# Optimization experiments

Measured on AMD Instinct MI355X. Metric: run time of the kernel, lower is better.

The kernel has to match this reference:

```python
import jax, jax.numpy as jnp
import numpy as np

B, J, D, H = 4096, 17, 512, 8
DK = D // H  # 64
NEG = jnp.float32(-9e15)


def _build_adj_mask():
    # Human3.6M 17-joint skeleton (parent indices), symmetric + self-loops,
    # matching SemGCN's adj>0 mask (adj_mx_from_edges adds identity).
    parents = np.array([-1, 0, 1, 2, 0, 4, 5, 0, 7, 8, 9, 8, 11, 12, 8, 14, 15])
    A = np.eye(J, dtype=np.float32)
    for c, p in enumerate(parents):
        if p >= 0:
            A[c, p] = 1.0
            A[p, c] = 1.0
    rows, cols = np.nonzero(A)
    return rows.astype(np.int32), cols.astype(np.int32)


def setup_inputs() -> dict:
    key = jax.random.key(0)
    ks = jax.random.split(key, 16)
    s = 0.02
    rows, cols = _build_adj_mask()
    return {
        "src": jax.random.normal(ks[0], (B, J, D), jnp.float32),
        # per-head Q/K/V Linears, stacked over heads: [H, D, DK]
        "Wq": jax.random.normal(ks[1], (H, D, DK), jnp.float32) * s,
        "bq": jnp.zeros((H, DK), jnp.float32),
        "Wk": jax.random.normal(ks[2], (H, D, DK), jnp.float32) * s,
        "bk": jnp.zeros((H, DK), jnp.float32),
        "Wv": jax.random.normal(ks[3], (H, D, DK), jnp.float32) * s,
        "bv": jnp.zeros((H, DK), jnp.float32),
        # output projection of MultiHeadAttention: [H*DK, D]
        "Wo": jax.random.normal(ks[4], (H * DK, D), jnp.float32) * s,
        "bo": jnp.zeros((D,), jnp.float32),
        "ln1_g": jnp.ones((D,), jnp.float32),
        "ln1_b": jnp.zeros((D,), jnp.float32),
        # SemGraphConv: two weight matrices [2, D, D], edge logits e, bias
        "W_gcn": jax.random.normal(ks[5], (2, D, D), jnp.float32) * s,
        "e_gcn": jax.random.normal(ks[6], (rows.shape[0],), jnp.float32),
        "b_gcn": jnp.zeros((D,), jnp.float32),
        "ln2_g": jnp.ones((D,), jnp.float32),
        "ln2_b": jnp.zeros((D,), jnp.float32),
        "mask_rows": jnp.asarray(rows),
        "mask_cols": jnp.asarray(cols),
    }


def _layernorm(x, g, b, eps=1e-5):
    mu = jnp.mean(x, axis=-1, keepdims=True)
    var = jnp.var(x, axis=-1, keepdims=True)
    return (x - mu) * jax.lax.rsqrt(var + eps) * g + b


def _forward(src, Wq, bq, Wk, bk, Wv, bv, Wo, bo, ln1_g, ln1_b,
             W_gcn, e_gcn, b_gcn, ln2_g, ln2_b, mask_rows, mask_cols):
    # --- multi-head attention (all heads vectorized) ---
    q = jnp.einsum('bjd,hde->bhje', src, Wq) + bq[None, :, None, :]
    k = jnp.einsum('bjd,hde->bhje', src, Wk) + bk[None, :, None, :]
    v = jnp.einsum('bjd,hde->bhje', src, Wv) + bv[None, :, None, :]
    scale = jnp.float32(DK) ** 0.5  # q.size(-1) ** 0.5
    att = jax.nn.softmax(jnp.einsum('bhje,bhke->bhjk', q, k) / scale, axis=-1)
    o = jnp.einsum('bhjk,bhke->bhje', att, v)          # [B,H,J,DK]
    o = o.transpose(0, 2, 1, 3).reshape(B, J, H * DK)  # concat over heads
    attn_out = o @ Wo + bo
    x = _layernorm(src + attn_out, ln1_g, ln1_b)

    # --- SemGraphConv ---
    h0 = x @ W_gcn[0]
    h1 = x @ W_gcn[1]
    logits = jnp.full((J, J), NEG, jnp.float32).at[mask_rows, mask_cols].set(e_gcn)
    A = jax.nn.softmax(logits, axis=1)                 # [J,J]
    I = jnp.eye(J, dtype=jnp.float32)
    gcn = jnp.einsum('jk,bkd->bjd', A * I, h0) + jnp.einsum('jk,bkd->bjd', A * (1.0 - I), h1)
    gcn = gcn + b_gcn
    return _layernorm(x + gcn, ln2_g, ln2_b)


def reference(src, Wq, bq, Wk, bk, Wv, bv, Wo, bo, ln1_g, ln1_b,
              W_gcn, e_gcn, b_gcn, ln2_g, ln2_b, mask_rows, mask_cols):
    return _forward(src, Wq, bq, Wk, bk, Wv, bv, Wo, bo, ln1_g, ln1_b,
                    W_gcn, e_gcn, b_gcn, ln2_g, ln2_b, mask_rows, mask_cols)
```

## Files before the change

kernel.cpp:

```cpp
#include <hip/hip_runtime.h>


typedef __attribute__((ext_vector_type(4))) float floatx4;
typedef __attribute__((ext_vector_type(8))) short short8;

#define AS1 __attribute__((address_space(1)))
#define AS3 __attribute__((address_space(3)))

__device__ __forceinline__ float bf2f(unsigned short u) {
  union { unsigned int i; float f; } x;
  x.i = ((unsigned int)u) << 16;
  return x.f;
}

__device__ __forceinline__ unsigned short f2bf(float f) {
  union { float f; unsigned int i; } x;
  x.f = f;
  unsigned int r = x.i + 0x7fffu + ((x.i >> 16) & 1u);
  return (unsigned short)(r >> 16);
}

__device__ __forceinline__ void unpack8(uint4 u, float* f) {
  unsigned int uu[4] = {u.x, u.y, u.z, u.w};
#pragma unroll
  for (int i = 0; i < 4; ++i) {
    f[2 * i]     = bf2f((unsigned short)(uu[i] & 0xffffu));
    f[2 * i + 1] = bf2f((unsigned short)(uu[i] >> 16));
  }
}

__device__ __forceinline__ uint4 pack8(const float* f) {
  unsigned int uu[4];
#pragma unroll
  for (int i = 0; i < 4; ++i)
    uu[i] = (unsigned int)f2bf(f[2 * i]) | ((unsigned int)f2bf(f[2 * i + 1]) << 16);
  uint4 u; u.x = uu[0]; u.y = uu[1]; u.z = uu[2]; u.w = uu[3];
  return u;
}

__device__ __forceinline__ float wave_sum(float v) {
#pragma unroll
  for (int m = 1; m < 64; m <<= 1) v += __shfl_xor(v, m, 64);
  return v;
}

__device__ __forceinline__ void gload_lds16(const unsigned short* g, AS3 char* l) {
  __builtin_amdgcn_global_load_lds((const AS1 void*)g, (AS3 void*)l, 16, 0, 0);
}

__global__ __launch_bounds__(256) void convert_src(
    const float* __restrict__ in, unsigned short* __restrict__ out) {
  const size_t i = ((size_t)blockIdx.x * 256 + threadIdx.x) * 8;
  const float4 a = *(const float4*)(in + i);
  const float4 b = *(const float4*)(in + i + 4);
  const float f[8] = {a.x, a.y, a.z, a.w, b.x, b.y, b.z, b.w};
  *(uint4*)(out + i) = pack8(f);
}

__device__ __forceinline__ void stgA(const unsigned short* a0, size_t gTh,
                                     AS3 char* L, int ldsW, int bb, int kt,
                                     int kh) {
  gload_lds16(a0 + gTh + kt * 64 + kh * 32,
              L + bb * 32768 + kh * 16384 + ldsW);
  gload_lds16(a0 + gTh + 65536 + kt * 64 + kh * 32,
              L + bb * 32768 + kh * 16384 + 8192 + ldsW);
}
__device__ __forceinline__ void stgB(const unsigned short* b0, size_t gTh,
                                     AS3 char* L, int ldsW, int bb, int kt,
                                     int kh) {
  gload_lds16(b0 + gTh + kt * 64 + kh * 32,
              L + 65536 + bb * 32768 + kh * 16384 + ldsW);
  gload_lds16(b0 + gTh + 65536 + kt * 64 + kh * 32,
              L + 65536 + bb * 32768 + kh * 16384 + 8192 + ldsW);
}

template <int BB>
__device__ __forceinline__ void kt_step(
    int kt, const char* Lr, AS3 char* L,
    const unsigned short* a0, const unsigned short* b0, size_t gTh, int ldsW,
    int aBase, int bBase, floatx4 (&acc)[8][4]) {
  constexpr int base = BB * 32768;
  short8 afL[4], afH[4], bf[4];

#pragma unroll
  for (int i = 0; i < 4; ++i)
    afL[i] = *(const short8*)(Lr + base + aBase + i * 1024);
#pragma unroll
  for (int j = 0; j < 4; ++j)
    bf[j] = *(const short8*)(Lr + base + bBase + j * 1024);
  if (kt < 7) stgA(a0, gTh, L, ldsW, BB ^ 1, kt + 1, 1);
  __builtin_amdgcn_s_barrier();
  asm volatile("s_waitcnt lgkmcnt(0)" ::: "memory");
  __builtin_amdgcn_sched_barrier(0);
  __builtin_amdgcn_s_setprio(1);
#pragma unroll
  for (int i = 0; i < 4; ++i)
#pragma unroll
    for (int j = 0; j < 4; ++j)
      acc[i][j] = __builtin_amdgcn_mfma_f32_16x16x32_bf16(afL[i], bf[j], acc[i][j], 0, 0, 0);
  __builtin_amdgcn_s_setprio(0);
  __builtin_amdgcn_s_barrier();

#pragma unroll
  for (int i = 0; i < 4; ++i)
    afH[i] = *(const short8*)(Lr + base + aBase + 4096 + i * 1024);
  if (kt < 7) stgB(b0, gTh, L, ldsW, BB ^ 1, kt + 1, 1);
  __builtin_amdgcn_s_barrier();
  asm volatile("s_waitcnt lgkmcnt(0)" ::: "memory");
  __builtin_amdgcn_sched_barrier(0);
  __builtin_amdgcn_s_setprio(1);
#pragma unroll
  for (int i = 0; i < 4; ++i)
#pragma unroll
    for (int j = 0; j < 4; ++j)
      acc[4 + i][j] = __builtin_amdgcn_mfma_f32_16x16x32_bf16(afH[i], bf[j], acc[4 + i][j], 0, 0, 0);
  __builtin_amdgcn_s_setprio(0);
  if (kt < 7) asm volatile("s_waitcnt vmcnt(8)" ::: "memory");
  else        asm volatile("s_waitcnt vmcnt(0)" ::: "memory");
  __builtin_amdgcn_sched_barrier(0);
  __builtin_amdgcn_s_barrier();

#pragma unroll
  for (int i = 0; i < 4; ++i)
    afL[i] = *(const short8*)(Lr + base + 16384 + aBase + i * 1024);
#pragma unroll
  for (int j = 0; j < 4; ++j)
    bf[j] = *(const short8*)(Lr + base + 16384 + bBase + j * 1024);
  if (kt < 6) stgA(a0, gTh, L, ldsW, BB, kt + 2, 0);
  __builtin_amdgcn_s_barrier();
  asm volatile("s_waitcnt lgkmcnt(0)" ::: "memory");
  __builtin_amdgcn_sched_barrier(0);
  __builtin_amdgcn_s_setprio(1);
#pragma unroll
  for (int i = 0; i < 4; ++i)
#pragma unroll
    for (int j = 0; j < 4; ++j)
      acc[i][j] = __builtin_amdgcn_mfma_f32_16x16x32_bf16(afL[i], bf[j], acc[i][j], 0, 0, 0);
  __builtin_amdgcn_s_setprio(0);
  __builtin_amdgcn_s_barrier();

#pragma unroll
  for (int i = 0; i < 4; ++i)
    afH[i] = *(const short8*)(Lr + base + 16384 + aBase + 4096 + i * 1024);
  if (kt < 6) stgB(b0, gTh, L, ldsW, BB, kt + 2, 0);
  __builtin_amdgcn_s_barrier();
  asm volatile("s_waitcnt lgkmcnt(0)" ::: "memory");
  __builtin_amdgcn_sched_barrier(0);
  __builtin_amdgcn_s_setprio(1);
#pragma unroll
  for (int i = 0; i < 4; ++i)
#pragma unroll
    for (int j = 0; j < 4; ++j)
      acc[4 + i][j] = __builtin_amdgcn_mfma_f32_16x16x32_bf16(afH[i], bf[j], acc[4 + i][j], 0, 0, 0);
  __builtin_amdgcn_s_setprio(0);
  if (kt < 6)       asm volatile("s_waitcnt vmcnt(8)" ::: "memory");
  else if (kt == 6) asm volatile("s_waitcnt vmcnt(4)" ::: "memory");
  __builtin_amdgcn_sched_barrier(0);
  __builtin_amdgcn_s_barrier();
}

__global__ __launch_bounds__(512, 2) void gemm_bt(
    const unsigned short* __restrict__ A,
    const unsigned short* __restrict__ BT,
    const float* __restrict__ bias,
    unsigned short* __restrict__ C, int N) {
  __shared__ char LDSR[131072];
  const int t = threadIdx.x;
  const int wave = t >> 6, lane = t & 63;
  const int wm = wave >> 2, wn = wave & 3;
  const int e = lane & 15, g = lane >> 4;

  const int nTN = N >> 8;
  const int q8 = gridDim.x >> 3;
  const int lin = ((int)blockIdx.x & 7) * q8 + ((int)blockIdx.x >> 3);
  const int tm = lin / nTN;
  const int tn = lin - tm * nTN;
  const long rowBase = (long)tm * 256;
  const long colBase = (long)tn * 256;

  const unsigned short* a0 = A + (size_t)rowBase * 512;
  const unsigned short* b0 = BT + (size_t)colBase * 512;

  const size_t gTh = (size_t)(t >> 2) * 512 +
                     (size_t)(((t & 3) ^ ((t >> 3) & 3))) * 8;
  AS3 char* L = (AS3 char*)LDSR;
  const int ldsW = wave * 1024;

  const int swz16 = ((g ^ ((e >> 1) & 3)) << 4);
  const char* Lr = LDSR;
  const int aBase = wm * 8192 + e * 64 + swz16;
  const int bBase = 65536 + wn * 4096 + e * 64 + swz16;

  floatx4 acc[8][4];
#pragma unroll
  for (int i = 0; i < 8; ++i)
#pragma unroll
    for (int j = 0; j < 4; ++j) acc[i][j] = (floatx4){0.f, 0.f, 0.f, 0.f};

  stgA(a0, gTh, L, ldsW, 0, 0, 0); stgB(b0, gTh, L, ldsW, 0, 0, 0);
  stgA(a0, gTh, L, ldsW, 0, 0, 1); stgB(b0, gTh, L, ldsW, 0, 0, 1);
  stgA(a0, gTh, L, ldsW, 1, 1, 0); stgB(b0, gTh, L, ldsW, 1, 1, 0);
  asm volatile("s_waitcnt vmcnt(8)" ::: "memory");
  __builtin_amdgcn_sched_barrier(0);
  __builtin_amdgcn_s_barrier();

#pragma unroll 1
  for (int ktp = 0; ktp < 4; ++ktp) {
    kt_step<0>(2 * ktp,     Lr, L, a0, b0, gTh, ldsW, aBase, bBase, acc);
    kt_step<1>(2 * ktp + 1, Lr, L, a0, b0, gTh, ldsW, aBase, bBase, acc);
  }

  asm volatile("s_waitcnt vmcnt(0) lgkmcnt(0)" ::: "memory");
  __builtin_amdgcn_sched_barrier(0);

  const int q4 = g << 2;
#pragma unroll
  for (int mf = 0; mf < 8; ++mf) {
    const long rowa = rowBase + wm * 128 + mf * 16 + q4;
#pragma unroll
    for (int nf = 0; nf < 4; ++nf) {
      const long col = colBase + wn * 64 + nf * 16 + e;
      const float badd = bias ? bias[col] : 0.f;
#pragma unroll
      for (int r = 0; r < 4; ++r)
        C[(size_t)(rowa + r) * N + col] = f2bf(acc[mf][nf][r] + badd);
    }
  }
}

__global__ __launch_bounds__(256) void attn_kernel(
    const unsigned short* __restrict__ qkv, unsigned short* __restrict__ o) {
  __shared__ unsigned short Vl[4][17][76];
  const int t = threadIdx.x;
  const int wave = t >> 6, lane = t & 63;
  const int wid = blockIdx.x * 4 + wave;
  const int b = wid >> 3, h = wid & 7;
  const int e = lane & 15, g = lane >> 4;

  const unsigned short* base = qkv + (size_t)b * 17 * 1536 + h * 64;

  unsigned short (*V)[76] = Vl[wave];
  for (int c = lane; c < 136; c += 64) {
    const int kk = c >> 3, e0 = (c & 7) << 3;
    const uint4 u = *(const uint4*)(base + (size_t)kk * 1536 + 1024 + e0);
    *(uint2*)&V[kk][e0]     = make_uint2(u.x, u.y);
    *(uint2*)&V[kk][e0 + 4] = make_uint2(u.z, u.w);
  }

  const int ko = g << 3;
  const unsigned short* qrow  = base + (size_t)e * 1536;
  const unsigned short* row16 = base + (size_t)16 * 1536;
  const short8 Q0  = *(const short8*)(qrow + ko);
  const short8 Q1  = *(const short8*)(qrow + 32 + ko);
  const short8 K0  = *(const short8*)(qrow + 512 + ko);
  const short8 K1  = *(const short8*)(qrow + 512 + 32 + ko);
  const short8 Qb0 = *(const short8*)(row16 + ko);
  const short8 Qb1 = *(const short8*)(row16 + 32 + ko);
  const short8 Kb0 = *(const short8*)(row16 + 512 + ko);
  const short8 Kb1 = *(const short8*)(row16 + 512 + 32 + ko);

  floatx4 sT[2][2];
#pragma unroll
  for (int i = 0; i < 2; ++i)
#pragma unroll
    for (int j = 0; j < 2; ++j) sT[i][j] = (floatx4){0.f, 0.f, 0.f, 0.f};
  sT[0][0] = __builtin_amdgcn_mfma_f32_16x16x32_bf16(K0, Q0, sT[0][0], 0, 0, 0);
  sT[0][0] = __builtin_amdgcn_mfma_f32_16x16x32_bf16(K1, Q1, sT[0][0], 0, 0, 0);
  sT[0][1] = __builtin_amdgcn_mfma_f32_16x16x32_bf16(K0, Qb0, sT[0][1], 0, 0, 0);
  sT[0][1] = __builtin_amdgcn_mfma_f32_16x16x32_bf16(K1, Qb1, sT[0][1], 0, 0, 0);
  sT[1][0] = __builtin_amdgcn_mfma_f32_16x16x32_bf16(Kb0, Q0, sT[1][0], 0, 0, 0);
  sT[1][0] = __builtin_amdgcn_mfma_f32_16x16x32_bf16(Kb1, Q1, sT[1][0], 0, 0, 0);
  sT[1][1] = __builtin_amdgcn_mfma_f32_16x16x32_bf16(Kb0, Qb0, sT[1][1], 0, 0, 0);
  sT[1][1] = __builtin_amdgcn_mfma_f32_16x16x32_bf16(Kb1, Qb1, sT[1][1], 0, 0, 0);

  short8 PA[2];
#pragma unroll
  for (int ni = 0; ni < 2; ++ni) {
    float v[4];
#pragma unroll
    for (int r = 0; r < 4; ++r) v[r] = sT[0][ni][r] * 0.125f;
    const float v16 = sT[1][ni][0] * 0.125f;
    float m = fmaxf(fmaxf(v[0], v[1]), fmaxf(v[2], v[3]));
    if (g == 0) m = fmaxf(m, v16);
    m = fmaxf(m, __shfl_xor(m, 16, 64));
    m = fmaxf(m, __shfl_xor(m, 32, 64));
    float p[4], sum = 0.f;
#pragma unroll
    for (int r = 0; r < 4; ++r) { p[r] = __expf(v[r] - m); sum += p[r]; }
    float p16 = (g == 0) ? __expf(v16 - m) : 0.f;
    sum += p16;
    sum += __shfl_xor(sum, 16, 64);
    sum += __shfl_xor(sum, 32, 64);
    const float inv = 1.f / sum;
#pragma unroll
    for (int r = 0; r < 4; ++r) p[r] *= inv;
    p16 *= inv;

    const unsigned int lo = (unsigned int)f2bf(p[0]) | ((unsigned int)f2bf(p[1]) << 16);
    const unsigned int hi = (unsigned int)f2bf(p[2]) | ((unsigned int)f2bf(p[3]) << 16);
    const unsigned int w16 = (unsigned int)f2bf(p16);

    const int colsrc = ni ? 0 : e;
    const int s0 = colsrc + ((g & 1) << 5);
    unsigned int w0 = __shfl(lo, s0, 64);
    unsigned int w1 = __shfl(hi, s0, 64);
    unsigned int w2 = __shfl(lo, s0 + 16, 64);
    unsigned int w3 = __shfl(hi, s0 + 16, 64);
    const unsigned int a16 = __shfl(w16, colsrc, 64);
    if (g == 2) { w0 = a16; w1 = 0; w2 = 0; w3 = 0; }
    if (g == 3) { w0 = 0; w1 = 0; w2 = 0; w3 = 0; }
    union { unsigned int u[4]; short8 s; } fa;
    fa.u[0] = w0; fa.u[1] = w1; fa.u[2] = w2; fa.u[3] = w3;
    PA[ni] = fa.s;
  }

  floatx4 o0[4], o1[4];
#pragma unroll
  for (int tt = 0; tt < 4; ++tt) {
    o0[tt] = (floatx4){0.f, 0.f, 0.f, 0.f};
    o1[tt] = (floatx4){0.f, 0.f, 0.f, 0.f};
  }
#pragma unroll
  for (int tt = 0; tt < 4; ++tt) {
    const int c = tt * 16 + e;
    union { unsigned int u[4]; short8 s; } fb;
#pragma unroll
    for (int i = 0; i < 4; ++i) {
      int ka = (g << 3) + 2 * i;
      int kb = ka + 1;
      if (ka > 16) ka = 16;
      if (kb > 16) kb = 16;
      fb.u[i] = (unsigned int)V[ka][c] | ((unsigned int)V[kb][c] << 16);
    }
    o0[tt] = __builtin_amdgcn_mfma_f32_16x16x32_bf16(PA[0], fb.s, o0[tt], 0, 0, 0);
    o1[tt] = __builtin_amdgcn_mfma_f32_16x16x32_bf16(PA[1], fb.s, o1[tt], 0, 0, 0);
  }

  unsigned short* ob = o + (size_t)b * 17 * 512 + h * 64;
#pragma unroll
  for (int tt = 0; tt < 4; ++tt)
#pragma unroll
    for (int r = 0; r < 4; ++r)
      ob[(size_t)(4 * g + r) * 512 + tt * 16 + e] = f2bf(o0[tt][r]);
  if (g == 0) {
#pragma unroll
    for (int tt = 0; tt < 4; ++tt)
      ob[(size_t)16 * 512 + tt * 16 + e] = f2bf(o1[tt][0]);
  }
}

__global__ __launch_bounds__(256) void ln_res_kernel(
    const float* __restrict__ a, const unsigned short* __restrict__ b,
    const float* __restrict__ g, const float* __restrict__ beta,
    unsigned short* __restrict__ out) {
  const long row = (long)blockIdx.x * 4 + (threadIdx.x >> 6);
  const int lane = threadIdx.x & 63;
  const int d0 = lane * 8;

  const float4 a0 = *(const float4*)(a + (size_t)row * 512 + d0);
  const float4 a1 = *(const float4*)(a + (size_t)row * 512 + d0 + 4);
  const float fa[8] = {a0.x, a0.y, a0.z, a0.w, a1.x, a1.y, a1.z, a1.w};
  float fb[8], vals[8];
  unpack8(*(const uint4*)(b + (size_t)row * 512 + d0), fb);
  float s = 0.f, s2 = 0.f;
#pragma unroll
  for (int i = 0; i < 8; ++i) {
    vals[i] = fa[i] + fb[i];
    s += vals[i];
    s2 += vals[i] * vals[i];
  }
  const float mean = wave_sum(s) * (1.f / 512.f);
  const float var = wave_sum(s2) * (1.f / 512.f) - mean * mean;
  const float rs = rsqrtf(var + 1e-5f);

  const float4 g0 = *(const float4*)(g + d0);
  const float4 g1 = *(const float4*)(g + d0 + 4);
  const float4 b0 = *(const float4*)(beta + d0);
  const float4 b1 = *(const float4*)(beta + d0 + 4);
  const float fg[8]  = {g0.x, g0.y, g0.z, g0.w, g1.x, g1.y, g1.z, g1.w};
  const float fbt[8] = {b0.x, b0.y, b0.z, b0.w, b1.x, b1.y, b1.z, b1.w};
  float y[8];
#pragma unroll
  for (int i = 0; i < 8; ++i) y[i] = (vals[i] - mean) * rs * fg[i] + fbt[i];
  *(uint4*)(out + (size_t)row * 512 + d0) = pack8(y);
}

__global__ __launch_bounds__(256) void gcn_ln_kernel(
    const unsigned short* __restrict__ x, const unsigned short* __restrict__ h01,
    const float* __restrict__ Adiag, const int* __restrict__ cnt,
    const int* __restrict__ nbrk, const float* __restrict__ nbrw,
    const float* __restrict__ bgcn,
    const float* __restrict__ g, const float* __restrict__ beta,
    float* __restrict__ out) {
  const long row = (long)blockIdx.x * 4 + (threadIdx.x >> 6);
  const int lane = threadIdx.x & 63;
  const int b = (int)(row / 17);
  const int j = (int)(row - (long)b * 17);
  const int d0 = lane * 8;

  float accv[8];
  {
    const float w = Adiag[j];
    float f[8];
    unpack8(*(const uint4*)(h01 + (size_t)row * 1024 + d0), f);
#pragma unroll
    for (int i = 0; i < 8; ++i) accv[i] = w * f[i];
  }
  const int c = cnt[j];
  for (int nb = 0; nb < c; ++nb) {
    const int kk = nbrk[j * 8 + nb];
    const float w = nbrw[j * 8 + nb];
    float f[8];
    unpack8(*(const uint4*)(h01 + ((size_t)b * 17 + kk) * 1024 + 512 + d0), f);
#pragma unroll
    for (int i = 0; i < 8; ++i) accv[i] += w * f[i];
  }

  float fx[8], vals[8];
  unpack8(*(const uint4*)(x + (size_t)row * 512 + d0), fx);
  const float4 bg0 = *(const float4*)(bgcn + d0);
  const float4 bg1 = *(const float4*)(bgcn + d0 + 4);
  const float fbg[8] = {bg0.x, bg0.y, bg0.z, bg0.w, bg1.x, bg1.y, bg1.z, bg1.w};
  float s = 0.f, s2 = 0.f;
#pragma unroll
  for (int i = 0; i < 8; ++i) {
    vals[i] = fx[i] + accv[i] + fbg[i];
    s += vals[i];
    s2 += vals[i] * vals[i];
  }
  const float mean = wave_sum(s) * (1.f / 512.f);
  const float var = wave_sum(s2) * (1.f / 512.f) - mean * mean;
  const float rs = rsqrtf(var + 1e-5f);

  const float4 g0 = *(const float4*)(g + d0);
  const float4 g1 = *(const float4*)(g + d0 + 4);
  const float4 bb0 = *(const float4*)(beta + d0);
  const float4 bb1 = *(const float4*)(beta + d0 + 4);
  const float fg[8]  = {g0.x, g0.y, g0.z, g0.w, g1.x, g1.y, g1.z, g1.w};
  const float fbt[8] = {bb0.x, bb0.y, bb0.z, bb0.w, bb1.x, bb1.y, bb1.z, bb1.w};
  float4 y0, y1;
  y0.x = (vals[0] - mean) * rs * fg[0] + fbt[0];
  y0.y = (vals[1] - mean) * rs * fg[1] + fbt[1];
  y0.z = (vals[2] - mean) * rs * fg[2] + fbt[2];
  y0.w = (vals[3] - mean) * rs * fg[3] + fbt[3];
  y1.x = (vals[4] - mean) * rs * fg[4] + fbt[4];
  y1.y = (vals[5] - mean) * rs * fg[5] + fbt[5];
  y1.z = (vals[6] - mean) * rs * fg[6] + fbt[6];
  y1.w = (vals[7] - mean) * rs * fg[7] + fbt[7];
  *(float4*)(out + (size_t)row * 512 + d0) = y0;
  *(float4*)(out + (size_t)row * 512 + d0 + 4) = y1;
}

__global__ __launch_bounds__(256) void prep_transpose(
    const float* __restrict__ Wq, const float* __restrict__ Wk,
    const float* __restrict__ Wv, const float* __restrict__ Wo,
    const float* __restrict__ Wg,
    unsigned short* __restrict__ WT1, unsigned short* __restrict__ WT2,
    unsigned short* __restrict__ WT3) {
  const int idx = blockIdx.x * 256 + threadIdx.x;
  if (idx < 786432) {
    const int n = idx >> 9, k = idx & 511;
    const int which = n >> 9, nn = n & 511;
    const int hh = nn >> 6, e = nn & 63;
    const float* W = (which == 0) ? Wq : (which == 1) ? Wk : Wv;
    WT1[idx] = f2bf(W[hh * 32768 + k * 64 + e]);
  } else if (idx < 786432 + 262144) {
    const int i2 = idx - 786432;
    const int n = i2 >> 9, k = i2 & 511;
    WT2[i2] = f2bf(Wo[k * 512 + n]);
  } else {
    const int i3 = idx - 1048576;
    const int n = i3 >> 9, k = i3 & 511;
    const int which = n >> 9, nn = n & 511;
    WT3[i3] = f2bf(Wg[which * 262144 + k * 512 + nn]);
  }
}

__global__ __launch_bounds__(256) void prep_small(
    const float* __restrict__ bq, const float* __restrict__ bk,
    const float* __restrict__ bv, const float* __restrict__ bo,
    const float* __restrict__ e, const int* __restrict__ rows,
    const int* __restrict__ cols, int nnz,
    float* __restrict__ bias1, float* __restrict__ bias2,
    float* __restrict__ Adiag, int* __restrict__ cnt,
    int* __restrict__ nbrk, float* __restrict__ nbrw) {
  const int t = threadIdx.x;
  for (int i = t; i < 1536; i += 256)
    bias1[i] = (i < 512) ? bq[i] : (i < 1024) ? bk[i - 512] : bv[i - 1024];
  for (int i = t; i < 512; i += 256) bias2[i] = bo[i];
  if (t < 17) {
    float m = -1e30f;
    for (int i = 0; i < nnz; ++i)
      if (rows[i] == t) m = fmaxf(m, e[i]);
    float s = 0.f;
    for (int i = 0; i < nnz; ++i)
      if (rows[i] == t) s += __expf(e[i] - m);
    const float inv = 1.f / s;
    int c = 0;
    for (int i = 0; i < nnz; ++i)
      if (rows[i] == t) {
        const float w = __expf(e[i] - m) * inv;
        const int kk = cols[i];
        if (kk == t) Adiag[t] = w;
        else { nbrk[t * 8 + c] = kk; nbrw[t * 8 + c] = w; ++c; }
      }
    cnt[t] = c;
  }
}

extern "C" void kernel_launch(void* const* d_in, const int* in_sizes, int n_in,
                              void* d_out, int out_size, void* d_ws, size_t ws_size,
                              hipStream_t stream) {
  const float* src = (const float*)d_in[0];
  const float* Wq  = (const float*)d_in[1];
  const float* bq  = (const float*)d_in[2];
  const float* Wk  = (const float*)d_in[3];
  const float* bk  = (const float*)d_in[4];
  const float* Wv  = (const float*)d_in[5];
  const float* bv  = (const float*)d_in[6];
  const float* Wo  = (const float*)d_in[7];
  const float* bo  = (const float*)d_in[8];
  const float* ln1g = (const float*)d_in[9];
  const float* ln1b = (const float*)d_in[10];
  const float* Wg  = (const float*)d_in[11];
  const float* eg  = (const float*)d_in[12];
  const float* bg  = (const float*)d_in[13];
  const float* ln2g = (const float*)d_in[14];
  const float* ln2b = (const float*)d_in[15];
  const int* mrows = (const int*)d_in[16];
  const int* mcols = (const int*)d_in[17];
  const int nnz = in_sizes[16];

  float* out = (float*)d_out;
  char* ws = (char*)d_ws;

  unsigned short* WT1 = (unsigned short*)(ws + 0x0000000);
  unsigned short* WT2 = (unsigned short*)(ws + 0x0180000);
  unsigned short* WT3 = (unsigned short*)(ws + 0x0200000);
  float* bias1 = (float*)(ws + 0x0300000);
  float* bias2 = (float*)(ws + 0x0302000);
  float* Adiag = (float*)(ws + 0x0303000);
  int* cnt     = (int*)(ws + 0x0303100);
  int* nbrk    = (int*)(ws + 0x0303200);
  float* nbrw  = (float*)(ws + 0x0303600);
  unsigned short* SRCB = (unsigned short*)(ws + 0x0400000);
  unsigned short* QKV  = (unsigned short*)(ws + 0x4800000);
  unsigned short* O    = (unsigned short*)(ws + 0x0400000);
  unsigned short* ATT  = (unsigned short*)(ws + 0x4800000);
  unsigned short* X    = (unsigned short*)(ws + 0x8C00000);
  unsigned short* H01  = (unsigned short*)(ws + 0x0400000);

  (void)n_in; (void)out_size; (void)ws_size;

  convert_src<<<17408, 256, 0, stream>>>(src, SRCB);
  prep_transpose<<<6144, 256, 0, stream>>>(Wq, Wk, Wv, Wo, Wg, WT1, WT2, WT3);
  prep_small<<<1, 256, 0, stream>>>(bq, bk, bv, bo, eg, mrows, mcols, nnz,
                                    bias1, bias2, Adiag, cnt, nbrk, nbrw);
  gemm_bt<<<1632, 512, 0, stream>>>(SRCB, WT1, bias1, QKV, 1536);
  attn_kernel<<<8192, 256, 0, stream>>>(QKV, O);
  gemm_bt<<<544, 512, 0, stream>>>(O, WT2, bias2, ATT, 512);
  ln_res_kernel<<<17408, 256, 0, stream>>>(src, ATT, ln1g, ln1b, X);
  gemm_bt<<<1088, 512, 0, stream>>>(X, WT3, nullptr, H01, 1024);
  gcn_ln_kernel<<<17408, 256, 0, stream>>>(X, H01, Adiag, cnt, nbrk, nbrw, bg,
                                           ln2g, ln2b, out);
}
```

Baseline: 795.1 us.

## Fuse output projection GEMM with residual add and LayerNorm; tile weight transpose

Adds a gemm_ln kernel in which each block computes a full 128x512 row tile of the output projection. It adds bias and the fp32 residual, reduces row statistics across waves through LDS, and writes normalized bf16 X directly. This removes the ATT intermediate round trip and the separate LayerNorm launch. Separately, the weight transpose now goes through a 64x64 LDS tile so both reads and writes are coalesced, replacing strided per-element gathers. The fused kernel uses about 120KB of LDS and a triple-buffered pipeline, and its epilogue reads src with a strided pattern, which may cost occupancy and bandwidth.

```diff
diff --git a/kernel.cpp b/kernel.cpp
--- a/kernel.cpp
+++ b/kernel.cpp
@@ -226,6 +226,162 @@
         C[(size_t)(rowa + r) * N + col] = f2bf(acc[mf][nf][r] + badd);
     }
   }
+}
+
+__global__ __launch_bounds__(512) void gemm_ln(
+    const unsigned short* __restrict__ A,
+    const unsigned short* __restrict__ BT,
+    const float* __restrict__ bias,
+    const float* __restrict__ srcf,
+    const float* __restrict__ g1, const float* __restrict__ b1,
+    unsigned short* __restrict__ X) {
+  __shared__ char LDSR[122880];
+  const int t = threadIdx.x;
+  const int w = t >> 6, lane = t & 63;
+  const int e = lane & 15, g = lane >> 4;
+
+  const int q8 = gridDim.x >> 3;
+  const int tm = ((int)blockIdx.x & 7) * q8 + ((int)blockIdx.x >> 3);
+  const long rowBase = (long)tm * 128;
+  const unsigned short* a0 = A + (size_t)rowBase * 512;
+
+  const size_t gOffA = (size_t)(t >> 2) * 512 +
+                       (size_t)(((t & 3) ^ ((t >> 3) & 3))) * 8;
+  size_t gOffB[4];
+#pragma unroll
+  for (int i = 0; i < 4; ++i) {
+    const int c = t + 512 * i;
+    gOffB[i] = (size_t)(c >> 2) * 512 + (size_t)(((c & 3) ^ ((c >> 3) & 3))) * 8;
+  }
+  AS3 char* L = (AS3 char*)LDSR;
+  const int ldsW = w * 1024;
+
+#define STG5(bb, kt)                                                         \
+  do {                                                                       \
+    gload_lds16(a0 + gOffA + (kt) * 32, L + (bb) * 40960 + ldsW);            \
+    gload_lds16(BT + gOffB[0] + (kt) * 32, L + (bb) * 40960 + 8192 + ldsW);  \
+    gload_lds16(BT + gOffB[1] + (kt) * 32,                                   \
+                L + (bb) * 40960 + 16384 + ldsW);                            \
+    gload_lds16(BT + gOffB[2] + (kt) * 32,                                   \
+                L + (bb) * 40960 + 24576 + ldsW);                            \
+    gload_lds16(BT + gOffB[3] + (kt) * 32,                                   \
+                L + (bb) * 40960 + 32768 + ldsW);                            \
+  } while (0)
+
+  const int swz16 = ((g ^ ((e >> 1) & 3)) << 4);
+  const char* Lr = LDSR;
+
+  floatx4 acc[8][4];
+#pragma unroll
+  for (int i = 0; i < 8; ++i)
+#pragma unroll
+    for (int j = 0; j < 4; ++j) acc[i][j] = (floatx4){0.f, 0.f, 0.f, 0.f};
+
+  STG5(0, 0);
+  STG5(1, 1);
+  asm volatile("s_waitcnt vmcnt(5)" ::: "memory");
+  __builtin_amdgcn_sched_barrier(0);
+  __builtin_amdgcn_s_barrier();
+
+#pragma unroll 1
+  for (int kt = 0; kt < 16; ++kt) {
+    const int bb = kt % 3;
+    if (kt + 2 < 16) STG5((kt + 2) % 3, kt + 2);
+
+    const int base = bb * 40960;
+    short8 af[8], bf4[4];
+#pragma unroll
+    for (int mf = 0; mf < 8; ++mf)
+      af[mf] = *(const short8*)(Lr + base + (16 * mf + e) * 64 + swz16);
+#pragma unroll
+    for (int nf = 0; nf < 4; ++nf)
+      bf4[nf] = *(const short8*)(Lr + base + 8192 +
+                                 (64 * w + 16 * nf + e) * 64 + swz16);
+#pragma unroll
+    for (int mf = 0; mf < 8; ++mf)
+#pragma unroll
+      for (int nf = 0; nf < 4; ++nf)
+        acc[mf][nf] = __builtin_amdgcn_mfma_f32_16x16x32_bf16(af[mf], bf4[nf], acc[mf][nf], 0, 0, 0);
+
+    if (kt == 15) break;
+    if (kt < 14) asm volatile("s_waitcnt vmcnt(5)" ::: "memory");
+    else         asm volatile("s_waitcnt vmcnt(0)" ::: "memory");
+    __builtin_amdgcn_sched_barrier(0);
+    __builtin_amdgcn_s_barrier();
+  }
+#undef STG5
+  __syncthreads();
+
+  float bb4[4], gg4[4], be4[4];
+#pragma unroll
+  for (int nf = 0; nf < 4; ++nf) {
+    const int col = 64 * w + 16 * nf + e;
+    bb4[nf] = bias[col];
+    gg4[nf] = g1[col];
+    be4[nf] = b1[col];
+  }
+#pragma unroll
+  for (int mf = 0; mf < 8; ++mf)
+#pragma unroll
+    for (int r = 0; r < 4; ++r) {
+      const long row = rowBase + 16 * mf + 4 * g + r;
+#pragma unroll
+      for (int nf = 0; nf < 4; ++nf)
+        acc[mf][nf][r] += bb4[nf] + srcf[(size_t)row * 512 + 64 * w + 16 * nf + e];
+    }
+
+  float* Ps  = (float*)LDSR;
+  float* Ps2 = (float*)(LDSR + 4608);
+#pragma unroll
+  for (int mf = 0; mf < 8; ++mf)
+#pragma unroll
+    for (int r = 0; r < 4; ++r) {
+      float s = 0.f, s2 = 0.f;
+#pragma unroll
+      for (int nf = 0; nf < 4; ++nf) {
+        const float v = acc[mf][nf][r];
+        s += v; s2 += v * v;
+      }
+#pragma unroll
+      for (int m = 1; m < 16; m <<= 1) {
+        s  += __shfl_xor(s,  m, 64);
+        s2 += __shfl_xor(s2, m, 64);
+      }
+      if (e == 0) {
+        const int rl = 16 * mf + 4 * g + r;
+        Ps[rl * 9 + w]  = s;
+        Ps2[rl * 9 + w] = s2;
+      }
+    }
+  __syncthreads();
+
+  float* St = (float*)(LDSR + 9216);
+  if (t < 128) {
+    float s = 0.f, s2 = 0.f;
+#pragma unroll
+    for (int ww = 0; ww < 8; ++ww) { s += Ps[t * 9 + ww]; s2 += Ps2[t * 9 + ww]; }
+    const float mean = s * (1.f / 512.f);
+    const float var = s2 * (1.f / 512.f) - mean * mean;
+    St[t] = mean;
+    St[128 + t] = rsqrtf(var + 1e-5f);
+  }
+  __syncthreads();
+
+#pragma unroll
+  for (int mf = 0; mf < 8; ++mf)
+#pragma unroll
+    for (int r = 0; r < 4; ++r) {
+      const int rl = 16 * mf + 4 * g + r;
+      const float mean = St[rl];
+      const float rs = St[128 + rl];
+      const long row = rowBase + rl;
+#pragma unroll
+      for (int nf = 0; nf < 4; ++nf) {
+        const int col = 64 * w + 16 * nf + e;
+        X[(size_t)row * 512 + col] =
+            f2bf((acc[mf][nf][r] - mean) * rs * gg4[nf] + be4[nf]);
+      }
+    }
 }
 
 __global__ __launch_bounds__(256) void attn_kernel(
@@ -347,42 +503,6 @@
     for (int tt = 0; tt < 4; ++tt)
       ob[(size_t)16 * 512 + tt * 16 + e] = f2bf(o1[tt][0]);
   }
-}
-
-__global__ __launch_bounds__(256) void ln_res_kernel(
-    const float* __restrict__ a, const unsigned short* __restrict__ b,
-    const float* __restrict__ g, const float* __restrict__ beta,
-    unsigned short* __restrict__ out) {
-  const long row = (long)blockIdx.x * 4 + (threadIdx.x >> 6);
-  const int lane = threadIdx.x & 63;
-  const int d0 = lane * 8;
-
-  const float4 a0 = *(const float4*)(a + (size_t)row * 512 + d0);
-  const float4 a1 = *(const float4*)(a + (size_t)row * 512 + d0 + 4);
-  const float fa[8] = {a0.x, a0.y, a0.z, a0.w, a1.x, a1.y, a1.z, a1.w};
-  float fb[8], vals[8];
-  unpack8(*(const uint4*)(b + (size_t)row * 512 + d0), fb);
-  float s = 0.f, s2 = 0.f;
-#pragma unroll
-  for (int i = 0; i < 8; ++i) {
-    vals[i] = fa[i] + fb[i];
-    s += vals[i];
-    s2 += vals[i] * vals[i];
-  }
-  const float mean = wave_sum(s) * (1.f / 512.f);
-  const float var = wave_sum(s2) * (1.f / 512.f) - mean * mean;
-  const float rs = rsqrtf(var + 1e-5f);
-
-  const float4 g0 = *(const float4*)(g + d0);
-  const float4 g1 = *(const float4*)(g + d0 + 4);
-  const float4 b0 = *(const float4*)(beta + d0);
-  const float4 b1 = *(const float4*)(beta + d0 + 4);
-  const float fg[8]  = {g0.x, g0.y, g0.z, g0.w, g1.x, g1.y, g1.z, g1.w};
-  const float fbt[8] = {b0.x, b0.y, b0.z, b0.w, b1.x, b1.y, b1.z, b1.w};
-  float y[8];
-#pragma unroll
-  for (int i = 0; i < 8; ++i) y[i] = (vals[i] - mean) * rs * fg[i] + fbt[i];
-  *(uint4*)(out + (size_t)row * 512 + d0) = pack8(y);
 }
 
 __global__ __launch_bounds__(256) void gcn_ln_kernel(
@@ -457,22 +577,53 @@
     const float* __restrict__ Wg,
     unsigned short* __restrict__ WT1, unsigned short* __restrict__ WT2,
     unsigned short* __restrict__ WT3) {
-  const int idx = blockIdx.x * 256 + threadIdx.x;
-  if (idx < 786432) {
-    const int n = idx >> 9, k = idx & 511;
-    const int which = n >> 9, nn = n & 511;
-    const int hh = nn >> 6, e = nn & 63;
+  __shared__ float T[64][65];
+  const int t = threadIdx.x;
+  const int bid = blockIdx.x;
+
+  const float* srcP;
+  int strideK, kBase, dstRowBase;
+  unsigned short* dst;
+  if (bid < 192) {
+    const int u = bid >> 3, kt8 = bid & 7;
+    const int which = u >> 3, hh = u & 7;
     const float* W = (which == 0) ? Wq : (which == 1) ? Wk : Wv;
-    WT1[idx] = f2bf(W[hh * 32768 + k * 64 + e]);
-  } else if (idx < 786432 + 262144) {
-    const int i2 = idx - 786432;
-    const int n = i2 >> 9, k = i2 & 511;
-    WT2[i2] = f2bf(Wo[k * 512 + n]);
+    srcP = W + hh * 32768 + kt8 * 64 * 64;
+    strideK = 64;
+    kBase = kt8 * 64;
+    dstRowBase = which * 512 + hh * 64;
+    dst = WT1;
+  } else if (bid < 256) {
+    const int t2 = bid - 192;
+    const int nt = t2 >> 3, kt8 = t2 & 7;
+    srcP = Wo + (size_t)kt8 * 64 * 512 + nt * 64;
+    strideK = 512;
+    kBase = kt8 * 64;
+    dstRowBase = nt * 64;
+    dst = WT2;
   } else {
-    const int i3 = idx - 1048576;
-    const int n = i3 >> 9, k = i3 & 511;
-    const int which = n >> 9, nn = n & 511;
-    WT3[i3] = f2bf(Wg[which * 262144 + k * 512 + nn]);
+    const int t3 = bid - 256;
+    const int which = t3 >> 6, r = t3 & 63;
+    const int nt = r >> 3, kt8 = r & 7;
+    srcP = Wg + (size_t)which * 262144 + (size_t)kt8 * 64 * 512 + nt * 64;
+    strideK = 512;
+    kBase = kt8 * 64;
+    dstRowBase = which * 512 + nt * 64;
+    dst = WT3;
+  }
+
+  const int r4 = t >> 6, cl = t & 63;
+#pragma unroll
+  for (int p = 0; p < 16; ++p) {
+    const int kl = p * 4 + r4;
+    T[kl][cl] = srcP[(size_t)kl * strideK + cl];
+  }
+  __syncthreads();
+#pragma unroll
+  for (int p = 0; p < 16; ++p) {
+    const int c2 = p * 4 + r4;
+    const int k2 = cl;
+    dst[(size_t)(dstRowBase + c2) * 512 + kBase + k2] = f2bf(T[k2][c2]);
   }
 }
 
@@ -546,20 +697,18 @@
   unsigned short* SRCB = (unsigned short*)(ws + 0x0400000);
   unsigned short* QKV  = (unsigned short*)(ws + 0x4800000);
   unsigned short* O    = (unsigned short*)(ws + 0x0400000);
-  unsigned short* ATT  = (unsigned short*)(ws + 0x4800000);
   unsigned short* X    = (unsigned short*)(ws + 0x8C00000);
   unsigned short* H01  = (unsigned short*)(ws + 0x0400000);
 
   (void)n_in; (void)out_size; (void)ws_size;
 
   convert_src<<<17408, 256, 0, stream>>>(src, SRCB);
-  prep_transpose<<<6144, 256, 0, stream>>>(Wq, Wk, Wv, Wo, Wg, WT1, WT2, WT3);
+  prep_transpose<<<384, 256, 0, stream>>>(Wq, Wk, Wv, Wo, Wg, WT1, WT2, WT3);
   prep_small<<<1, 256, 0, stream>>>(bq, bk, bv, bo, eg, mrows, mcols, nnz,
                                     bias1, bias2, Adiag, cnt, nbrk, nbrw);
   gemm_bt<<<1632, 512, 0, stream>>>(SRCB, WT1, bias1, QKV, 1536);
   attn_kernel<<<8192, 256, 0, stream>>>(QKV, O);
-  gemm_bt<<<544, 512, 0, stream>>>(O, WT2, bias2, ATT, 512);
-  ln_res_kernel<<<17408, 256, 0, stream>>>(src, ATT, ln1g, ln1b, X);
+  gemm_ln<<<544, 512, 0, stream>>>(O, WT2, bias2, src, ln1g, ln1b, X);
   gemm_bt<<<1088, 512, 0, stream>>>(X, WT3, nullptr, H01, 1024);
   gcn_ln_kernel<<<17408, 256, 0, stream>>>(X, H01, Adiag, cnt, nbrk, nbrw, bg,
                                            ln2g, ln2b, out);
```

After: 929.6 us. 16.9% more time.
